# Kernel tuning notes

Hardware: AMD Instinct MI355X
Metric: run time of the kernel (lower is better)

## Reference

```python
import jax, jax.numpy as jnp
import numpy as np

EPS = 1e-8
HIDDEN = 200


def _dsmall(n, d):
    # torch: d = d*(d>eps) + eps*(d<=eps); n/d
    return n / jnp.where(d > EPS, d, EPS)


def _mp_match(v1, v2, w):
    # v1: (B,S,H); v2: (B,S,H) or (B,H); w: (L,H) -> (B,S,L)
    wt = w.T[None, None]                      # (1,1,H,L)
    a = v1[..., None] * wt                    # (B,S,H,L)
    if v2.ndim == 2:
        v2 = jnp.broadcast_to(v2[:, None, :], v1.shape)
    b = v2[..., None] * wt                    # (B,S,H,L)
    dot = jnp.sum(a * b, axis=2)
    na = jnp.linalg.norm(a, axis=2)
    nb = jnp.linalg.norm(b, axis=2)
    return dot / jnp.maximum(na * nb, EPS)    # cosine_similarity over H


def _mp_pairwise(v1, v2, w):
    # v1: (B,S1,H); v2: (B,S2,H); w: (L,H) -> (B,S1,S2,L)
    a = v1[:, None] * w[None, :, None]        # (B,L,S1,H)
    b = v2[:, None] * w[None, :, None]        # (B,L,S2,H)
    na = jnp.linalg.norm(a, axis=3, keepdims=True)   # (B,L,S1,1)
    nb = jnp.linalg.norm(b, axis=3, keepdims=True)   # (B,L,S2,1)
    n = jnp.einsum('blph,blqh->blpq', a, b)
    d = na * jnp.swapaxes(nb, 2, 3)
    return jnp.transpose(_dsmall(n, d), (0, 2, 3, 1))


def _attention(v1, v2):
    # cosine-similarity matrix (B,S1,S2)
    n1 = jnp.linalg.norm(v1, axis=2, keepdims=True)           # (B,S1,1)
    n2 = jnp.linalg.norm(v2, axis=2, keepdims=True)           # (B,S2,1)
    a = jnp.einsum('bph,bqh->bpq', v1, v2)
    return _dsmall(a, n1 * jnp.swapaxes(n2, 1, 2))


def _matching(con_p, con_h, w1, w2, w3, w4, w5, w6, w7, w8):
    p_fw, p_bw = con_p[..., :HIDDEN], con_p[..., HIDDEN:]
    h_fw, h_bw = con_h[..., :HIDDEN], con_h[..., HIDDEN:]

    # 1) full matching
    mv_p_full_fw = _mp_match(p_fw, h_fw[:, -1, :], w1)
    mv_p_full_bw = _mp_match(p_bw, h_bw[:, 0, :], w2)
    mv_h_full_fw = _mp_match(h_fw, p_fw[:, -1, :], w1)
    mv_h_full_bw = _mp_match(h_bw, p_bw[:, 0, :], w2)

    # 2) maxpooling matching
    mv_max_fw = _mp_pairwise(p_fw, h_fw, w3)  # (B,S1,S2,L)
    mv_max_bw = _mp_pairwise(p_bw, h_bw, w4)
    mv_p_max_fw = jnp.max(mv_max_fw, axis=2)
    mv_p_max_bw = jnp.max(mv_max_bw, axis=2)
    mv_h_max_fw = jnp.max(mv_max_fw, axis=1)
    mv_h_max_bw = jnp.max(mv_max_bw, axis=1)

    # 3) attentive matching (mean)
    att_fw = _attention(p_fw, h_fw)           # (B,S1,S2)
    att_bw = _attention(p_bw, h_bw)

    # sum of att_h over dim 2 is a matmul (same math, no (B,S1,S2,H) tensor)
    att_h_sum_fw = jnp.einsum('bpq,bqh->bph', att_fw, h_fw)
    att_h_sum_bw = jnp.einsum('bpq,bqh->bph', att_bw, h_bw)
    att_p_sum_fw = jnp.einsum('bpq,bph->bqh', att_fw, p_fw)
    att_p_sum_bw = jnp.einsum('bpq,bph->bqh', att_bw, p_bw)

    att_mean_h_fw = _dsmall(att_h_sum_fw, jnp.sum(att_fw, axis=2, keepdims=True))
    att_mean_h_bw = _dsmall(att_h_sum_bw, jnp.sum(att_bw, axis=2, keepdims=True))
    att_mean_p_fw = _dsmall(att_p_sum_fw, jnp.swapaxes(jnp.sum(att_fw, axis=1, keepdims=True), 1, 2))
    att_mean_p_bw = _dsmall(att_p_sum_bw, jnp.swapaxes(jnp.sum(att_bw, axis=1, keepdims=True), 1, 2))

    mv_p_att_mean_fw = _mp_match(p_fw, att_mean_h_fw, w5)
    mv_p_att_mean_bw = _mp_match(p_bw, att_mean_h_bw, w6)
    mv_h_att_mean_fw = _mp_match(h_fw, att_mean_p_fw, w5)
    mv_h_att_mean_bw = _mp_match(h_bw, att_mean_p_bw, w6)

    # 4) max-attentive matching (needs full (B,S1,S2,H) broadcast for the max)
    att_h_fw = h_fw[:, None, :, :] * att_fw[:, :, :, None]   # (B,S1,S2,H)
    att_h_bw = h_bw[:, None, :, :] * att_bw[:, :, :, None]
    att_p_fw = p_fw[:, :, None, :] * att_fw[:, :, :, None]
    att_p_bw = p_bw[:, :, None, :] * att_bw[:, :, :, None]

    att_max_h_fw = jnp.max(att_h_fw, axis=2)                 # (B,S1,H)
    att_max_h_bw = jnp.max(att_h_bw, axis=2)
    att_max_p_fw = jnp.max(att_p_fw, axis=1)                 # (B,S2,H)
    att_max_p_bw = jnp.max(att_p_bw, axis=1)

    mv_p_att_max_fw = _mp_match(p_fw, att_max_h_fw, w7)
    mv_p_att_max_bw = _mp_match(p_bw, att_max_h_bw, w8)
    mv_h_att_max_fw = _mp_match(h_fw, att_max_p_fw, w7)
    mv_h_att_max_bw = _mp_match(h_bw, att_max_p_bw, w8)

    mv_p = jnp.concatenate([mv_p_full_fw, mv_p_max_fw, mv_p_att_mean_fw, mv_p_att_max_fw,
                            mv_p_full_bw, mv_p_max_bw, mv_p_att_mean_bw, mv_p_att_max_bw], axis=2)
    mv_h = jnp.concatenate([mv_h_full_fw, mv_h_max_fw, mv_h_att_mean_fw, mv_h_att_max_fw,
                            mv_h_full_bw, mv_h_max_bw, mv_h_att_mean_bw, mv_h_att_max_bw], axis=2)
    # dropout is identity in inference mode
    return mv_p, mv_h


def setup_inputs() -> dict:
    key = jax.random.key(0)
    ks = jax.random.split(key, 10)
    B, S, H, L = 32, 64, HIDDEN, 20
    w_std = np.sqrt(2.0 / H)  # kaiming_normal fan_in
    inp = {
        'con_p': jax.random.normal(ks[0], (B, S, 2 * H), dtype=jnp.float32),
        'con_h': jax.random.normal(ks[1], (B, S, 2 * H), dtype=jnp.float32),
    }
    for i in range(8):
        inp[f'mp_w{i+1}'] = jax.random.normal(ks[2 + i], (L, H), dtype=jnp.float32) * w_std
    return inp


def reference(con_p, con_h, mp_w1, mp_w2, mp_w3, mp_w4, mp_w5, mp_w6, mp_w7, mp_w8):
    return _matching(con_p, con_h, mp_w1, mp_w2, mp_w3, mp_w4, mp_w5, mp_w6, mp_w7, mp_w8)
```

## Files before the change

kernel.cpp:

```cpp
#include <hip/hip_runtime.h>
#include <hip/hip_bf16.h>
#include <math.h>

#define EPS 1e-8f
#define BB 32
#define SS 64
#define HH 200
#define LL 20
#define KP 224
#define KST 232
#define MST 204
#define SST 68

typedef short bf16x8 __attribute__((ext_vector_type(8)));
typedef float f32x4 __attribute__((ext_vector_type(4)));

__device__ inline float bf2f(short u) {
    union { unsigned int i; float f; } v;
    v.i = ((unsigned int)(unsigned short)u) << 16;
    return v.f;
}


__global__ __launch_bounds__(512) void fused1_kernel(
        const float* __restrict__ conp, const float* __restrict__ conh,
        const float* __restrict__ w3, const float* __restrict__ w4,
        float* __restrict__ wn, float* __restrict__ meanv, float* __restrict__ maxv) {
    __shared__ __align__(16) float smem[13440];
    int t = threadIdx.x;

    if (blockIdx.x < 256) {
        float* w2L = smem;
        float* x2L = smem + 4080;
        int wnb = blockIdx.x;
        int sh = wnb & 1, sdb = wnb >> 1;
        int b = sdb & 31, sd = sdb >> 5;
        int dir = sd & 1, side = sd >> 1;
        const float* wsrc = dir ? w4 : w3;
        for (int e = t; e < LL * 25; e += 512) {
            int l = e / 25, c = e % 25, h0 = c * 8;
            float4 u0 = *(const float4*)(wsrc + l * HH + h0);
            float4 u1 = *(const float4*)(wsrc + l * HH + h0 + 4);
            *(float4*)&w2L[l * MST + h0]     = make_float4(u0.x * u0.x, u0.y * u0.y, u0.z * u0.z, u0.w * u0.w);
            *(float4*)&w2L[l * MST + h0 + 4] = make_float4(u1.x * u1.x, u1.y * u1.y, u1.z * u1.z, u1.w * u1.w);
        }
        const float* xbase = side ? conh : conp;
        for (int e = t; e < 32 * 25; e += 512) {
            int s_ = e / 25, c = e % 25, h0 = c * 8;
            const float* xp = xbase + (b * SS + sh * 32 + s_) * (2 * HH) + dir * HH + h0;
            float4 u0 = *(const float4*)xp;
            float4 u1 = *(const float4*)(xp + 4);
            *(float4*)&x2L[s_ * MST + h0]     = make_float4(u0.x * u0.x, u0.y * u0.y, u0.z * u0.z, u0.w * u0.w);
            *(float4*)&x2L[s_ * MST + h0 + 4] = make_float4(u1.x * u1.x, u1.y * u1.y, u1.z * u1.z, u1.w * u1.w);
        }
        __syncthreads();
        for (int o = t; o < 32 * LL; o += 512) {
            int s_ = o / LL, l = o % LL;
            const float4* xp = (const float4*)&x2L[s_ * MST];
            const float4* wp = (const float4*)&w2L[l * MST];
            float a0 = 0.f, a1 = 0.f, a2 = 0.f, a3 = 0.f;
            for (int h4 = 0; h4 < 50; ++h4) {
                float4 x = xp[h4]; float4 w = wp[h4];
                a0 = fmaf(x.x, w.x, a0); a1 = fmaf(x.y, w.y, a1);
                a2 = fmaf(x.z, w.z, a2); a3 = fmaf(x.w, w.w, a3);
            }
            wn[((sd * BB + b) * SS + sh * 32 + s_) * LL + l] = sqrtf(a0 + a1 + a2 + a3);
        }
    } else {
        __hip_bfloat16* AT = (__hip_bfloat16*)smem;
        __hip_bfloat16* BT = (__hip_bfloat16*)(smem + 3712);
        float* S_L  = smem + 3712 + 7424;
        float* nrmA = S_L + 32 * SST;
        float* nrmB = nrmA + 32;
        float* dsum = nrmB + 64;

        int blk = blockIdx.x - 256;
        int sh = blk & 1;
        int sdb = blk >> 1;
        int b = sdb & 31, sd = sdb >> 5;
        int dir = sd & 1, side = sd >> 1;

        if (t < 32) nrmA[t] = 0.f;
        if (t < 64) nrmB[t] = 0.f;
        __syncthreads();

        const float* selfb = side ? conh : conp;
        const float* oppb  = side ? conp : conh;

        for (int e = t; e < 32 * 28; e += 512) {
            int sl = e / 28, ck = e % 28, k = ck * 8;
            __align__(16) __hip_bfloat16 r8[8];
            if (k < HH) {
                const float* xp = selfb + (b * SS + sh * 32 + sl) * (2 * HH) + dir * HH + k;
                float xv[8];
                *(float4*)&xv[0] = *(const float4*)xp; *(float4*)&xv[4] = *(const float4*)(xp + 4);
                float ss = 0.f;
#pragma unroll
                for (int i = 0; i < 8; ++i) { r8[i] = __float2bfloat16(xv[i]); ss = fmaf(xv[i], xv[i], ss); }
                atomicAdd(&nrmA[sl], ss);
            } else {
#pragma unroll
                for (int i = 0; i < 8; ++i) r8[i] = __float2bfloat16(0.f);
            }
            *(bf16x8*)&AT[sl * KST + k] = *(bf16x8*)r8;
        }
        for (int e = t; e < 64 * 28; e += 512) {
            int rw = e / 28, ck = e % 28, k = ck * 8;
            __align__(16) __hip_bfloat16 r8[8];
            if (k < HH) {
                const float* xp = oppb + (b * SS + rw) * (2 * HH) + dir * HH + k;
                float xv[8];
                *(float4*)&xv[0] = *(const float4*)xp; *(float4*)&xv[4] = *(const float4*)(xp + 4);
                float ss = 0.f;
#pragma unroll
                for (int i = 0; i < 8; ++i) { r8[i] = __float2bfloat16(xv[i]); ss = fmaf(xv[i], xv[i], ss); }
                atomicAdd(&nrmB[rw], ss);
            } else {
#pragma unroll
                for (int i = 0; i < 8; ++i) r8[i] = __float2bfloat16(0.f);
            }
            *(bf16x8*)&BT[rw * KST + k] = *(bf16x8*)r8;
        }
        __syncthreads();

        int wv_ = __builtin_amdgcn_readfirstlane(t >> 6);
        int lane = t & 63;
        int q = lane >> 4, c = lane & 15;
        int rt = wv_ & 1, ct = wv_ >> 1;

        f32x4 acc = (f32x4){0.f, 0.f, 0.f, 0.f};
        for (int ks = 0; ks < 7; ++ks) {
            int kb = ks * 32 + q * 8;
            bf16x8 af  = *(const bf16x8*)&AT[(rt * 16 + c) * KST + kb];
            bf16x8 bf_ = *(const bf16x8*)&BT[(ct * 16 + c) * KST + kb];
            acc = __builtin_amdgcn_mfma_f32_16x16x32_bf16(af, bf_, acc, 0, 0, 0);
        }
        {
            int col = ct * 16 + c;
            float no = sqrtf(nrmB[col]);
#pragma unroll
            for (int r = 0; r < 4; ++r) {
                int row = rt * 16 + q * 4 + r;
                float ns = sqrtf(nrmA[row]);
                S_L[row * SST + col] = acc[r] / fmaxf(ns * no, EPS);
            }
        }
        __syncthreads();

        if (t < 32) {
            float sm = 0.f;
            for (int k = 0; k < 64; ++k) sm += S_L[t * SST + k];
            dsum[t] = fmaxf(sm, EPS);
        }
        __syncthreads();

        for (int e = t; e < 32 * 25; e += 512) {
            int s = e / 25, hc = e % 25, h0 = hc * 8;
            float dsv = dsum[s];
            float ms[8], mx[8];
#pragma unroll
            for (int i = 0; i < 8; ++i) { ms[i] = 0.f; mx[i] = -INFINITY; }
            for (int k = 0; k < 64; ++k) {
                float a = S_L[s * SST + k];
                bf16x8 ov = *(const bf16x8*)&BT[k * KST + h0];
#pragma unroll
                for (int i = 0; i < 8; ++i) {
                    float tt = a * bf2f(ov[i]);
                    ms[i] += tt;
                    mx[i] = fmaxf(mx[i], tt);
                }
            }
            int obase = ((sd * BB + b) * SS + sh * 32 + s) * HH + h0;
#pragma unroll
            for (int i = 0; i < 8; ++i) ms[i] /= dsv;
            *(float4*)&meanv[obase]     = *(float4*)&ms[0];
            *(float4*)&meanv[obase + 4] = *(float4*)&ms[4];
            *(float4*)&maxv[obase]      = *(float4*)&mx[0];
            *(float4*)&maxv[obase + 4]  = *(float4*)&mx[4];
        }
    }
}

__global__ __launch_bounds__(256) void fused2_kernel(
        const float* __restrict__ conp, const float* __restrict__ conh,
        const float* __restrict__ meanv, const float* __restrict__ maxv,
        const float* __restrict__ w1, const float* __restrict__ w2,
        const float* __restrict__ w3, const float* __restrict__ w4,
        const float* __restrict__ w5, const float* __restrict__ w6,
        const float* __restrict__ w7, const float* __restrict__ w8,
        const float* __restrict__ wn, float* __restrict__ out) {
    __shared__ __align__(16) float smem[15104];
    int t = threadIdx.x;

    if (blockIdx.x < 768) {
        __hip_bfloat16* AT = (__hip_bfloat16*)smem;
        __hip_bfloat16* BT = (__hip_bfloat16*)(smem + 11136);
        int blk = blockIdx.x;
        int sh = blk & 1;
        int r_ = blk >> 1;
        int m = r_ % 3;
        int sdb = r_ / 3;
        int b = sdb & 31, sd = sdb >> 5;
        int dir = sd & 1, side = sd >> 1;

        const float* wsrc = (m == 0) ? (dir ? w2 : w1)
                          : (m == 1) ? (dir ? w6 : w5)
                                     : (dir ? w8 : w7);
        const float* xbase = side ? conh : conp;
        const float* opp   = side ? conp : conh;
        int fidx = dir ? 0 : (SS - 1);
        const float* fvr = opp + (b * SS + fidx) * (2 * HH) + dir * HH;

        for (int e = t; e < 32 * 28; e += 256) {
            int sl = e / 28, ck = e % 28;
            int k = ck * 8;
            int s = sh * 32 + sl;
            __align__(16) __hip_bfloat16 r0[8], r1[8], r2[8];
            if (k < HH) {
                const float* xp = xbase + (b * SS + s) * (2 * HH) + dir * HH + k;
                const float* yp = (m == 0) ? (fvr + k)
                                : ((m == 1 ? meanv : maxv) + ((sd * BB + b) * SS + s) * HH + k);
                float xv[8], yv[8];
                *(float4*)&xv[0] = *(const float4*)xp; *(float4*)&xv[4] = *(const float4*)(xp + 4);
                *(float4*)&yv[0] = *(const float4*)yp; *(float4*)&yv[4] = *(const float4*)(yp + 4);
#pragma unroll
                for (int i = 0; i < 8; ++i) {
                    r0[i] = __float2bfloat16(xv[i] * xv[i]);
                    r1[i] = __float2bfloat16(xv[i] * yv[i]);
                    r2[i] = __float2bfloat16(yv[i] * yv[i]);
                }
            } else {
#pragma unroll
                for (int i = 0; i < 8; ++i) {
                    r0[i] = __float2bfloat16(0.f); r1[i] = __float2bfloat16(0.f); r2[i] = __float2bfloat16(0.f);
                }
            }
            *(bf16x8*)&AT[(0 * 32 + sl) * KST + k] = *(bf16x8*)r0;
            *(bf16x8*)&AT[(1 * 32 + sl) * KST + k] = *(bf16x8*)r1;
            *(bf16x8*)&AT[(2 * 32 + sl) * KST + k] = *(bf16x8*)r2;
        }
        for (int e = t; e < 32 * 28; e += 256) {
            int l = e / 28, ck = e % 28;
            int k = ck * 8;
            __align__(16) __hip_bfloat16 wr[8];
            if (l < LL && k < HH) {
                const float* wp = wsrc + l * HH + k;
                float wv[8];
                *(float4*)&wv[0] = *(const float4*)wp; *(float4*)&wv[4] = *(const float4*)(wp + 4);
#pragma unroll
                for (int i = 0; i < 8; ++i) wr[i] = __float2bfloat16(wv[i] * wv[i]);
            } else {
#pragma unroll
                for (int i = 0; i < 8; ++i) wr[i] = __float2bfloat16(0.f);
            }
            *(bf16x8*)&BT[l * KST + k] = *(bf16x8*)wr;
        }
        __syncthreads();

        int wv_ = __builtin_amdgcn_readfirstlane(t >> 6);
        int lane = t & 63;
        int q = lane >> 4, c = lane & 15;
        int slh = wv_ >> 1, ntile = wv_ & 1;

        f32x4 accA = (f32x4){0.f, 0.f, 0.f, 0.f};
        f32x4 accD = (f32x4){0.f, 0.f, 0.f, 0.f};
        f32x4 accB = (f32x4){0.f, 0.f, 0.f, 0.f};
        for (int ks = 0; ks < 7; ++ks) {
            int kb = ks * 32 + q * 8;
            bf16x8 bf = *(const bf16x8*)&BT[(ntile * 16 + c) * KST + kb];
            bf16x8 a0 = *(const bf16x8*)&AT[(0 * 32 + slh * 16 + c) * KST + kb];
            bf16x8 a1 = *(const bf16x8*)&AT[(1 * 32 + slh * 16 + c) * KST + kb];
            bf16x8 a2 = *(const bf16x8*)&AT[(2 * 32 + slh * 16 + c) * KST + kb];
            accA = __builtin_amdgcn_mfma_f32_16x16x32_bf16(a0, bf, accA, 0, 0, 0);
            accD = __builtin_amdgcn_mfma_f32_16x16x32_bf16(a1, bf, accD, 0, 0, 0);
            accB = __builtin_amdgcn_mfma_f32_16x16x32_bf16(a2, bf, accB, 0, 0, 0);
        }

        int l = ntile * 16 + c;
        if (l < LL) {
            int chunk = (m == 0) ? 0 : (m == 1) ? 40 : 60;
#pragma unroll
            for (int r = 0; r < 4; ++r) {
                int s = sh * 32 + slh * 16 + q * 4 + r;
                float cosv = accD[r] / fmaxf(sqrtf(accA[r] * accB[r]), EPS);
                out[side * (BB * SS * 160) + (b * SS + s) * 160 + dir * 80 + chunk + l] = cosv;
            }
        }
    } else {
        __hip_bfloat16* AT = (__hip_bfloat16*)smem;
        __hip_bfloat16* BT = (__hip_bfloat16*)(smem + 7424);
        float* cmL = smem + 14848;
        int blk = blockIdx.x - 768;
        int l = blk % LL; int db = blk / LL; int b = db & 31; int dir = db >> 5;

        const float* wrow = (dir ? w4 : w3) + l * HH;
        const float* Ag = conp + dir * HH;
        const float* Bg = conh + dir * HH;

        for (int e = t; e < 64 * 28; e += 256) {
            int m = e / 28, ck = e - m * 28;
            int k = ck * 8;
            __align__(16) __hip_bfloat16 at8[8];
            __align__(16) __hip_bfloat16 bt8[8];
            if (k < HH) {
                const float* ap = Ag + (b * SS + m) * (2 * HH) + k;
                const float* bp = Bg + (b * SS + m) * (2 * HH) + k;
                const float* wp = wrow + k;
                float4 a0 = *(const float4*)ap, a1 = *(const float4*)(ap + 4);
                float4 b0 = *(const float4*)bp, b1 = *(const float4*)(bp + 4);
                float4 w0 = *(const float4*)wp, w1 = *(const float4*)(wp + 4);
                at8[0] = __float2bfloat16(a0.x * w0.x); at8[1] = __float2bfloat16(a0.y * w0.y);
                at8[2] = __float2bfloat16(a0.z * w0.z); at8[3] = __float2bfloat16(a0.w * w0.w);
                at8[4] = __float2bfloat16(a1.x * w1.x); at8[5] = __float2bfloat16(a1.y * w1.y);
                at8[6] = __float2bfloat16(a1.z * w1.z); at8[7] = __float2bfloat16(a1.w * w1.w);
                bt8[0] = __float2bfloat16(b0.x * w0.x); bt8[1] = __float2bfloat16(b0.y * w0.y);
                bt8[2] = __float2bfloat16(b0.z * w0.z); bt8[3] = __float2bfloat16(b0.w * w0.w);
                bt8[4] = __float2bfloat16(b1.x * w1.x); bt8[5] = __float2bfloat16(b1.y * w1.y);
                bt8[6] = __float2bfloat16(b1.z * w1.z); bt8[7] = __float2bfloat16(b1.w * w1.w);
            } else {
#pragma unroll
                for (int ii = 0; ii < 8; ++ii) { at8[ii] = __float2bfloat16(0.f); bt8[ii] = __float2bfloat16(0.f); }
            }
            *(bf16x8*)&AT[m * KST + k] = *(bf16x8*)at8;
            *(bf16x8*)&BT[m * KST + k] = *(bf16x8*)bt8;
        }
        __syncthreads();

        int wv_ = __builtin_amdgcn_readfirstlane(t >> 6);
        int lane = t & 63;
        int q = lane >> 4, c = lane & 15;
        int m0 = wv_ * 16;

        f32x4 acc[4];
#pragma unroll
        for (int ct = 0; ct < 4; ++ct) acc[ct] = (f32x4){0.f, 0.f, 0.f, 0.f};

        for (int ks = 0; ks < 7; ++ks) {
            int kb = ks * 32 + q * 8;
            bf16x8 af = *(const bf16x8*)&AT[(m0 + c) * KST + kb];
#pragma unroll
            for (int ct = 0; ct < 4; ++ct) {
                bf16x8 bf_ = *(const bf16x8*)&BT[(ct * 16 + c) * KST + kb];
                acc[ct] = __builtin_amdgcn_mfma_f32_16x16x32_bf16(af, bf_, acc[ct], 0, 0, 0);
            }
        }

        float na[4], nb[4];
#pragma unroll
        for (int r = 0; r < 4; ++r) {
            int i = m0 + q * 4 + r;
            na[r] = wn[(((0 * 2 + dir) * BB + b) * SS + i) * LL + l];
        }
#pragma unroll
        for (int ct = 0; ct < 4; ++ct) {
            int j = ct * 16 + c;
            nb[ct] = wn[(((1 * 2 + dir) * BB + b) * SS + j) * LL + l];
        }

        float rowm[4] = {-INFINITY, -INFINITY, -INFINITY, -INFINITY};
        float colm[4] = {-INFINITY, -INFINITY, -INFINITY, -INFINITY};
#pragma unroll
        for (int ct = 0; ct < 4; ++ct) {
#pragma unroll
            for (int r = 0; r < 4; ++r) {
                float cv = acc[ct][r] / fmaxf(na[r] * nb[ct], EPS);
                rowm[r] = fmaxf(rowm[r], cv);
                colm[ct] = fmaxf(colm[ct], cv);
            }
        }

#pragma unroll
        for (int r = 0; r < 4; ++r) {
            float v = rowm[r];
            v = fmaxf(v, __shfl_xor(v, 1, 64));
            v = fmaxf(v, __shfl_xor(v, 2, 64));
            v = fmaxf(v, __shfl_xor(v, 4, 64));
            v = fmaxf(v, __shfl_xor(v, 8, 64));
            rowm[r] = v;
        }
        if (c == 0) {
#pragma unroll
            for (int r = 0; r < 4; ++r) {
                int i = m0 + q * 4 + r;
                out[(b * SS + i) * 160 + dir * 80 + 20 + l] = rowm[r];
            }
        }

#pragma unroll
        for (int ct = 0; ct < 4; ++ct) {
            float v = colm[ct];
            v = fmaxf(v, __shfl_xor(v, 16, 64));
            v = fmaxf(v, __shfl_xor(v, 32, 64));
            colm[ct] = v;
        }
        if (q == 0) {
#pragma unroll
            for (int ct = 0; ct < 4; ++ct) cmL[wv_ * 64 + ct * 16 + c] = colm[ct];
        }
        __syncthreads();
        if (t < 64) {
            float m = fmaxf(fmaxf(cmL[t], cmL[64 + t]), fmaxf(cmL[128 + t], cmL[192 + t]));
            out[BB * SS * 160 + (b * SS + t) * 160 + dir * 80 + 20 + l] = m;
        }
    }
}

extern "C" void kernel_launch(void* const* d_in, const int* in_sizes, int n_in,
                              void* d_out, int out_size, void* d_ws, size_t ws_size,
                              hipStream_t stream) {
    const float* conp = (const float*)d_in[0];
    const float* conh = (const float*)d_in[1];
    const float* w1 = (const float*)d_in[2];
    const float* w2 = (const float*)d_in[3];
    const float* w3 = (const float*)d_in[4];
    const float* w4 = (const float*)d_in[5];
    const float* w5 = (const float*)d_in[6];
    const float* w6 = (const float*)d_in[7];
    const float* w7 = (const float*)d_in[8];
    const float* w8 = (const float*)d_in[9];
    float* out = (float*)d_out;
    float* ws  = (float*)d_ws;

    float* wn     = ws;
    float* meanv  = wn + 4 * BB * SS * LL;
    float* maxv   = meanv + 4 * BB * SS * HH;

    fused1_kernel<<<512, 512, 0, stream>>>(conp, conh, w3, w4, wn, meanv, maxv);
    fused2_kernel<<<2048, 256, 0, stream>>>(conp, conh, meanv, maxv,
                                            w1, w2, w3, w4, w5, w6, w7, w8, wn, out);
}
```

Baseline: 123.6 us.

## Fuse both kernels into one, keeping attention vectors in shared memory

Merges the two launches into a single kernel. The attention mean and max vectors now stay in LDS and feed the full, mean and max-attentive multi-perspective matches within the same block, instead of going through a global workspace. The weighted norms for the pairwise max-pooling path are now accumulated inline with LDS atomics, which removes the separate norm-computation blocks. This drops one launch and the global round trip, but LDS use grows to about 108KB per block, which cuts occupancy, and half the waves sit idle during the MFMA phases.

```diff
diff --git a/kernel.cpp b/kernel.cpp
--- a/kernel.cpp
+++ b/kernel.cpp
@@ -7,10 +7,9 @@
 #define SS 64
 #define HH 200
 #define LL 20
-#define KP 224
 #define KST 232
-#define MST 204
 #define SST 68
+#define MHS 200
 
 typedef short bf16x8 __attribute__((ext_vector_type(8)));
 typedef float f32x4 __attribute__((ext_vector_type(4)));
@@ -21,71 +20,39 @@
     return v.f;
 }
 
-
-__global__ __launch_bounds__(512) void fused1_kernel(
+__global__ __launch_bounds__(512) void fused_all_kernel(
         const float* __restrict__ conp, const float* __restrict__ conh,
+        const float* __restrict__ w1, const float* __restrict__ w2,
         const float* __restrict__ w3, const float* __restrict__ w4,
-        float* __restrict__ wn, float* __restrict__ meanv, float* __restrict__ maxv) {
-    __shared__ __align__(16) float smem[13440];
+        const float* __restrict__ w5, const float* __restrict__ w6,
+        const float* __restrict__ w7, const float* __restrict__ w8,
+        float* __restrict__ out) {
+    __shared__ __align__(16) float smem[27648];
     int t = threadIdx.x;
 
     if (blockIdx.x < 256) {
-        float* w2L = smem;
-        float* x2L = smem + 4080;
-        int wnb = blockIdx.x;
-        int sh = wnb & 1, sdb = wnb >> 1;
-        int b = sdb & 31, sd = sdb >> 5;
-        int dir = sd & 1, side = sd >> 1;
-        const float* wsrc = dir ? w4 : w3;
-        for (int e = t; e < LL * 25; e += 512) {
-            int l = e / 25, c = e % 25, h0 = c * 8;
-            float4 u0 = *(const float4*)(wsrc + l * HH + h0);
-            float4 u1 = *(const float4*)(wsrc + l * HH + h0 + 4);
-            *(float4*)&w2L[l * MST + h0]     = make_float4(u0.x * u0.x, u0.y * u0.y, u0.z * u0.z, u0.w * u0.w);
-            *(float4*)&w2L[l * MST + h0 + 4] = make_float4(u1.x * u1.x, u1.y * u1.y, u1.z * u1.z, u1.w * u1.w);
-        }
-        const float* xbase = side ? conh : conp;
-        for (int e = t; e < 32 * 25; e += 512) {
-            int s_ = e / 25, c = e % 25, h0 = c * 8;
-            const float* xp = xbase + (b * SS + sh * 32 + s_) * (2 * HH) + dir * HH + h0;
-            float4 u0 = *(const float4*)xp;
-            float4 u1 = *(const float4*)(xp + 4);
-            *(float4*)&x2L[s_ * MST + h0]     = make_float4(u0.x * u0.x, u0.y * u0.y, u0.z * u0.z, u0.w * u0.w);
-            *(float4*)&x2L[s_ * MST + h0 + 4] = make_float4(u1.x * u1.x, u1.y * u1.y, u1.z * u1.z, u1.w * u1.w);
-        }
-        __syncthreads();
-        for (int o = t; o < 32 * LL; o += 512) {
-            int s_ = o / LL, l = o % LL;
-            const float4* xp = (const float4*)&x2L[s_ * MST];
-            const float4* wp = (const float4*)&w2L[l * MST];
-            float a0 = 0.f, a1 = 0.f, a2 = 0.f, a3 = 0.f;
-            for (int h4 = 0; h4 < 50; ++h4) {
-                float4 x = xp[h4]; float4 w = wp[h4];
-                a0 = fmaf(x.x, w.x, a0); a1 = fmaf(x.y, w.y, a1);
-                a2 = fmaf(x.z, w.z, a2); a3 = fmaf(x.w, w.w, a3);
-            }
-            wn[((sd * BB + b) * SS + sh * 32 + s_) * LL + l] = sqrtf(a0 + a1 + a2 + a3);
-        }
-    } else {
         __hip_bfloat16* AT = (__hip_bfloat16*)smem;
         __hip_bfloat16* BT = (__hip_bfloat16*)(smem + 3712);
-        float* S_L  = smem + 3712 + 7424;
-        float* nrmA = S_L + 32 * SST;
+        float* S_L  = smem + 11136;
+        float* nrmA = smem + 13312;
         float* nrmB = nrmA + 32;
         float* dsum = nrmB + 64;
-
-        int blk = blockIdx.x - 256;
+        __hip_bfloat16* PB = (__hip_bfloat16*)smem;
+        __hip_bfloat16* WB = (__hip_bfloat16*)(smem + 11136);
+        float* meanL = smem + 14848;
+        float* maxL  = smem + 21248;
+
+        int blk = blockIdx.x;
         int sh = blk & 1;
         int sdb = blk >> 1;
         int b = sdb & 31, sd = sdb >> 5;
         int dir = sd & 1, side = sd >> 1;
+        const float* selfb = side ? conh : conp;
+        const float* oppb  = side ? conp : conh;
 
         if (t < 32) nrmA[t] = 0.f;
         if (t < 64) nrmB[t] = 0.f;
         __syncthreads();
-
-        const float* selfb = side ? conh : conp;
-        const float* oppb  = side ? conp : conh;
 
         for (int e = t; e < 32 * 28; e += 512) {
             int sl = e / 28, ck = e % 28, k = ck * 8;
@@ -126,16 +93,16 @@
         int wv_ = __builtin_amdgcn_readfirstlane(t >> 6);
         int lane = t & 63;
         int q = lane >> 4, c = lane & 15;
-        int rt = wv_ & 1, ct = wv_ >> 1;
-
-        f32x4 acc = (f32x4){0.f, 0.f, 0.f, 0.f};
-        for (int ks = 0; ks < 7; ++ks) {
-            int kb = ks * 32 + q * 8;
-            bf16x8 af  = *(const bf16x8*)&AT[(rt * 16 + c) * KST + kb];
-            bf16x8 bf_ = *(const bf16x8*)&BT[(ct * 16 + c) * KST + kb];
-            acc = __builtin_amdgcn_mfma_f32_16x16x32_bf16(af, bf_, acc, 0, 0, 0);
-        }
+
         {
+            int rt = wv_ & 1, ct = wv_ >> 1;
+            f32x4 acc = (f32x4){0.f, 0.f, 0.f, 0.f};
+            for (int ks = 0; ks < 7; ++ks) {
+                int kb = ks * 32 + q * 8;
+                bf16x8 af  = *(const bf16x8*)&AT[(rt * 16 + c) * KST + kb];
+                bf16x8 bf_ = *(const bf16x8*)&BT[(ct * 16 + c) * KST + kb];
+                acc = __builtin_amdgcn_mfma_f32_16x16x32_bf16(af, bf_, acc, 0, 0, 0);
+            }
             int col = ct * 16 + c;
             float no = sqrtf(nrmB[col]);
 #pragma unroll
@@ -170,134 +137,116 @@
                     mx[i] = fmaxf(mx[i], tt);
                 }
             }
-            int obase = ((sd * BB + b) * SS + sh * 32 + s) * HH + h0;
 #pragma unroll
             for (int i = 0; i < 8; ++i) ms[i] /= dsv;
-            *(float4*)&meanv[obase]     = *(float4*)&ms[0];
-            *(float4*)&meanv[obase + 4] = *(float4*)&ms[4];
-            *(float4*)&maxv[obase]      = *(float4*)&mx[0];
-            *(float4*)&maxv[obase + 4]  = *(float4*)&mx[4];
-        }
-    }
-}
-
-__global__ __launch_bounds__(256) void fused2_kernel(
-        const float* __restrict__ conp, const float* __restrict__ conh,
-        const float* __restrict__ meanv, const float* __restrict__ maxv,
-        const float* __restrict__ w1, const float* __restrict__ w2,
-        const float* __restrict__ w3, const float* __restrict__ w4,
-        const float* __restrict__ w5, const float* __restrict__ w6,
-        const float* __restrict__ w7, const float* __restrict__ w8,
-        const float* __restrict__ wn, float* __restrict__ out) {
-    __shared__ __align__(16) float smem[15104];
-    int t = threadIdx.x;
-
-    if (blockIdx.x < 768) {
-        __hip_bfloat16* AT = (__hip_bfloat16*)smem;
-        __hip_bfloat16* BT = (__hip_bfloat16*)(smem + 11136);
-        int blk = blockIdx.x;
-        int sh = blk & 1;
-        int r_ = blk >> 1;
-        int m = r_ % 3;
-        int sdb = r_ / 3;
-        int b = sdb & 31, sd = sdb >> 5;
-        int dir = sd & 1, side = sd >> 1;
-
-        const float* wsrc = (m == 0) ? (dir ? w2 : w1)
-                          : (m == 1) ? (dir ? w6 : w5)
-                                     : (dir ? w8 : w7);
-        const float* xbase = side ? conh : conp;
-        const float* opp   = side ? conp : conh;
+            *(float4*)&meanL[s * MHS + h0]     = *(float4*)&ms[0];
+            *(float4*)&meanL[s * MHS + h0 + 4] = *(float4*)&ms[4];
+            *(float4*)&maxL[s * MHS + h0]      = *(float4*)&mx[0];
+            *(float4*)&maxL[s * MHS + h0 + 4]  = *(float4*)&mx[4];
+        }
+        __syncthreads();
+
         int fidx = dir ? 0 : (SS - 1);
-        const float* fvr = opp + (b * SS + fidx) * (2 * HH) + dir * HH;
-
-        for (int e = t; e < 32 * 28; e += 256) {
-            int sl = e / 28, ck = e % 28;
-            int k = ck * 8;
-            int s = sh * 32 + sl;
-            __align__(16) __hip_bfloat16 r0[8], r1[8], r2[8];
-            if (k < HH) {
-                const float* xp = xbase + (b * SS + s) * (2 * HH) + dir * HH + k;
-                const float* yp = (m == 0) ? (fvr + k)
-                                : ((m == 1 ? meanv : maxv) + ((sd * BB + b) * SS + s) * HH + k);
-                float xv[8], yv[8];
-                *(float4*)&xv[0] = *(const float4*)xp; *(float4*)&xv[4] = *(const float4*)(xp + 4);
-                *(float4*)&yv[0] = *(const float4*)yp; *(float4*)&yv[4] = *(const float4*)(yp + 4);
-#pragma unroll
-                for (int i = 0; i < 8; ++i) {
-                    r0[i] = __float2bfloat16(xv[i] * xv[i]);
-                    r1[i] = __float2bfloat16(xv[i] * yv[i]);
-                    r2[i] = __float2bfloat16(yv[i] * yv[i]);
-                }
-            } else {
-#pragma unroll
-                for (int i = 0; i < 8; ++i) {
-                    r0[i] = __float2bfloat16(0.f); r1[i] = __float2bfloat16(0.f); r2[i] = __float2bfloat16(0.f);
-                }
-            }
-            *(bf16x8*)&AT[(0 * 32 + sl) * KST + k] = *(bf16x8*)r0;
-            *(bf16x8*)&AT[(1 * 32 + sl) * KST + k] = *(bf16x8*)r1;
-            *(bf16x8*)&AT[(2 * 32 + sl) * KST + k] = *(bf16x8*)r2;
-        }
-        for (int e = t; e < 32 * 28; e += 256) {
-            int l = e / 28, ck = e % 28;
-            int k = ck * 8;
-            __align__(16) __hip_bfloat16 wr[8];
-            if (l < LL && k < HH) {
-                const float* wp = wsrc + l * HH + k;
-                float wv[8];
-                *(float4*)&wv[0] = *(const float4*)wp; *(float4*)&wv[4] = *(const float4*)(wp + 4);
-#pragma unroll
-                for (int i = 0; i < 8; ++i) wr[i] = __float2bfloat16(wv[i] * wv[i]);
-            } else {
-#pragma unroll
-                for (int i = 0; i < 8; ++i) wr[i] = __float2bfloat16(0.f);
-            }
-            *(bf16x8*)&BT[l * KST + k] = *(bf16x8*)wr;
-        }
-        __syncthreads();
-
-        int wv_ = __builtin_amdgcn_readfirstlane(t >> 6);
-        int lane = t & 63;
-        int q = lane >> 4, c = lane & 15;
-        int slh = wv_ >> 1, ntile = wv_ & 1;
-
-        f32x4 accA = (f32x4){0.f, 0.f, 0.f, 0.f};
-        f32x4 accD = (f32x4){0.f, 0.f, 0.f, 0.f};
-        f32x4 accB = (f32x4){0.f, 0.f, 0.f, 0.f};
-        for (int ks = 0; ks < 7; ++ks) {
-            int kb = ks * 32 + q * 8;
-            bf16x8 bf = *(const bf16x8*)&BT[(ntile * 16 + c) * KST + kb];
-            bf16x8 a0 = *(const bf16x8*)&AT[(0 * 32 + slh * 16 + c) * KST + kb];
-            bf16x8 a1 = *(const bf16x8*)&AT[(1 * 32 + slh * 16 + c) * KST + kb];
-            bf16x8 a2 = *(const bf16x8*)&AT[(2 * 32 + slh * 16 + c) * KST + kb];
-            accA = __builtin_amdgcn_mfma_f32_16x16x32_bf16(a0, bf, accA, 0, 0, 0);
-            accD = __builtin_amdgcn_mfma_f32_16x16x32_bf16(a1, bf, accD, 0, 0, 0);
-            accB = __builtin_amdgcn_mfma_f32_16x16x32_bf16(a2, bf, accB, 0, 0, 0);
-        }
-
-        int l = ntile * 16 + c;
-        if (l < LL) {
-            int chunk = (m == 0) ? 0 : (m == 1) ? 40 : 60;
-#pragma unroll
-            for (int r = 0; r < 4; ++r) {
-                int s = sh * 32 + slh * 16 + q * 4 + r;
-                float cosv = accD[r] / fmaxf(sqrtf(accA[r] * accB[r]), EPS);
-                out[side * (BB * SS * 160) + (b * SS + s) * 160 + dir * 80 + chunk + l] = cosv;
-            }
+        const float* fvr = oppb + (b * SS + fidx) * (2 * HH) + dir * HH;
+        for (int m = 0; m < 3; ++m) {
+            const float* wsrc = (m == 0) ? (dir ? w2 : w1)
+                              : (m == 1) ? (dir ? w6 : w5)
+                                         : (dir ? w8 : w7);
+            for (int e = t; e < 32 * 28; e += 512) {
+                int sl = e / 28, ck = e % 28, k = ck * 8;
+                __align__(16) __hip_bfloat16 r0[8], r1[8], r2[8];
+                if (k < HH) {
+                    const float* xp = selfb + (b * SS + sh * 32 + sl) * (2 * HH) + dir * HH + k;
+                    float xv[8], yv[8];
+                    *(float4*)&xv[0] = *(const float4*)xp; *(float4*)&xv[4] = *(const float4*)(xp + 4);
+                    if (m == 0) {
+                        *(float4*)&yv[0] = *(const float4*)(fvr + k);
+                        *(float4*)&yv[4] = *(const float4*)(fvr + k + 4);
+                    } else {
+                        const float* yL = (m == 1 ? meanL : maxL) + sl * MHS + k;
+                        *(float4*)&yv[0] = *(const float4*)yL;
+                        *(float4*)&yv[4] = *(const float4*)(yL + 4);
+                    }
+#pragma unroll
+                    for (int i = 0; i < 8; ++i) {
+                        if (m == 0) r0[i] = __float2bfloat16(xv[i] * xv[i]);
+                        r1[i] = __float2bfloat16(xv[i] * yv[i]);
+                        r2[i] = __float2bfloat16(yv[i] * yv[i]);
+                    }
+                } else {
+#pragma unroll
+                    for (int i = 0; i < 8; ++i) {
+                        r0[i] = __float2bfloat16(0.f);
+                        r1[i] = __float2bfloat16(0.f);
+                        r2[i] = __float2bfloat16(0.f);
+                    }
+                }
+                if (m == 0) *(bf16x8*)&PB[(0 * 32 + sl) * KST + k] = *(bf16x8*)r0;
+                *(bf16x8*)&PB[(1 * 32 + sl) * KST + k] = *(bf16x8*)r1;
+                *(bf16x8*)&PB[(2 * 32 + sl) * KST + k] = *(bf16x8*)r2;
+            }
+            for (int e = t; e < 32 * 28; e += 512) {
+                int l_ = e / 28, ck = e % 28, k = ck * 8;
+                __align__(16) __hip_bfloat16 wr[8];
+                if (l_ < LL && k < HH) {
+                    const float* wp = wsrc + l_ * HH + k;
+                    float wv[8];
+                    *(float4*)&wv[0] = *(const float4*)wp; *(float4*)&wv[4] = *(const float4*)(wp + 4);
+#pragma unroll
+                    for (int i = 0; i < 8; ++i) wr[i] = __float2bfloat16(wv[i] * wv[i]);
+                } else {
+#pragma unroll
+                    for (int i = 0; i < 8; ++i) wr[i] = __float2bfloat16(0.f);
+                }
+                *(bf16x8*)&WB[l_ * KST + k] = *(bf16x8*)wr;
+            }
+            __syncthreads();
+
+            if (wv_ < 4) {
+                int slh = wv_ >> 1, ntile = wv_ & 1;
+                f32x4 accA = (f32x4){0.f, 0.f, 0.f, 0.f};
+                f32x4 accD = (f32x4){0.f, 0.f, 0.f, 0.f};
+                f32x4 accB = (f32x4){0.f, 0.f, 0.f, 0.f};
+                for (int ks = 0; ks < 7; ++ks) {
+                    int kb = ks * 32 + q * 8;
+                    bf16x8 bfw = *(const bf16x8*)&WB[(ntile * 16 + c) * KST + kb];
+                    bf16x8 a0 = *(const bf16x8*)&PB[(0 * 32 + slh * 16 + c) * KST + kb];
+                    bf16x8 a1 = *(const bf16x8*)&PB[(1 * 32 + slh * 16 + c) * KST + kb];
+                    bf16x8 a2 = *(const bf16x8*)&PB[(2 * 32 + slh * 16 + c) * KST + kb];
+                    accA = __builtin_amdgcn_mfma_f32_16x16x32_bf16(a0, bfw, accA, 0, 0, 0);
+                    accD = __builtin_amdgcn_mfma_f32_16x16x32_bf16(a1, bfw, accD, 0, 0, 0);
+                    accB = __builtin_amdgcn_mfma_f32_16x16x32_bf16(a2, bfw, accB, 0, 0, 0);
+                }
+                int l_ = ntile * 16 + c;
+                if (l_ < LL) {
+                    int chunk = (m == 0) ? 0 : (m == 1) ? 40 : 60;
+#pragma unroll
+                    for (int r = 0; r < 4; ++r) {
+                        int s = sh * 32 + slh * 16 + q * 4 + r;
+                        float cosv = accD[r] / fmaxf(sqrtf(accA[r] * accB[r]), EPS);
+                        out[side * (BB * SS * 160) + (b * SS + s) * 160 + dir * 80 + chunk + l_] = cosv;
+                    }
+                }
+            }
+            if (m < 2) __syncthreads();
         }
     } else {
         __hip_bfloat16* AT = (__hip_bfloat16*)smem;
         __hip_bfloat16* BT = (__hip_bfloat16*)(smem + 7424);
         float* cmL = smem + 14848;
-        int blk = blockIdx.x - 768;
+        float* nA  = smem + 15104;
+        float* nB  = smem + 15168;
+        int blk = blockIdx.x - 256;
         int l = blk % LL; int db = blk / LL; int b = db & 31; int dir = db >> 5;
 
         const float* wrow = (dir ? w4 : w3) + l * HH;
         const float* Ag = conp + dir * HH;
         const float* Bg = conh + dir * HH;
 
-        for (int e = t; e < 64 * 28; e += 256) {
+        if (t < 64) { nA[t] = 0.f; nB[t] = 0.f; }
+        __syncthreads();
+
+        for (int e = t; e < 64 * 28; e += 512) {
             int m = e / 28, ck = e - m * 28;
             int k = ck * 8;
             __align__(16) __hip_bfloat16 at8[8];
@@ -306,17 +255,22 @@
                 const float* ap = Ag + (b * SS + m) * (2 * HH) + k;
                 const float* bp = Bg + (b * SS + m) * (2 * HH) + k;
                 const float* wp = wrow + k;
-                float4 a0 = *(const float4*)ap, a1 = *(const float4*)(ap + 4);
-                float4 b0 = *(const float4*)bp, b1 = *(const float4*)(bp + 4);
-                float4 w0 = *(const float4*)wp, w1 = *(const float4*)(wp + 4);
-                at8[0] = __float2bfloat16(a0.x * w0.x); at8[1] = __float2bfloat16(a0.y * w0.y);
-                at8[2] = __float2bfloat16(a0.z * w0.z); at8[3] = __float2bfloat16(a0.w * w0.w);
-                at8[4] = __float2bfloat16(a1.x * w1.x); at8[5] = __float2bfloat16(a1.y * w1.y);
-                at8[6] = __float2bfloat16(a1.z * w1.z); at8[7] = __float2bfloat16(a1.w * w1.w);
-                bt8[0] = __float2bfloat16(b0.x * w0.x); bt8[1] = __float2bfloat16(b0.y * w0.y);
-                bt8[2] = __float2bfloat16(b0.z * w0.z); bt8[3] = __float2bfloat16(b0.w * w0.w);
-                bt8[4] = __float2bfloat16(b1.x * w1.x); bt8[5] = __float2bfloat16(b1.y * w1.y);
-                bt8[6] = __float2bfloat16(b1.z * w1.z); bt8[7] = __float2bfloat16(b1.w * w1.w);
+                float av[8], bv[8], wvv[8];
+                *(float4*)&av[0]  = *(const float4*)ap; *(float4*)&av[4]  = *(const float4*)(ap + 4);
+                *(float4*)&bv[0]  = *(const float4*)bp; *(float4*)&bv[4]  = *(const float4*)(bp + 4);
+                *(float4*)&wvv[0] = *(const float4*)wp; *(float4*)&wvv[4] = *(const float4*)(wp + 4);
+                float ssa = 0.f, ssb = 0.f;
+#pragma unroll
+                for (int i = 0; i < 8; ++i) {
+                    float aw = av[i] * wvv[i];
+                    float bw = bv[i] * wvv[i];
+                    at8[i] = __float2bfloat16(aw);
+                    bt8[i] = __float2bfloat16(bw);
+                    ssa = fmaf(aw, aw, ssa);
+                    ssb = fmaf(bw, bw, ssb);
+                }
+                atomicAdd(&nA[m], ssa);
+                atomicAdd(&nB[m], ssb);
             } else {
 #pragma unroll
                 for (int ii = 0; ii < 8; ++ii) { at8[ii] = __float2bfloat16(0.f); bt8[ii] = __float2bfloat16(0.f); }
@@ -329,78 +283,73 @@
         int wv_ = __builtin_amdgcn_readfirstlane(t >> 6);
         int lane = t & 63;
         int q = lane >> 4, c = lane & 15;
-        int m0 = wv_ * 16;
-
-        f32x4 acc[4];
-#pragma unroll
-        for (int ct = 0; ct < 4; ++ct) acc[ct] = (f32x4){0.f, 0.f, 0.f, 0.f};
-
-        for (int ks = 0; ks < 7; ++ks) {
-            int kb = ks * 32 + q * 8;
-            bf16x8 af = *(const bf16x8*)&AT[(m0 + c) * KST + kb];
+
+        if (wv_ < 4) {
+            int m0 = wv_ * 16;
+            f32x4 acc[4];
+#pragma unroll
+            for (int ct = 0; ct < 4; ++ct) acc[ct] = (f32x4){0.f, 0.f, 0.f, 0.f};
+            for (int ks = 0; ks < 7; ++ks) {
+                int kb = ks * 32 + q * 8;
+                bf16x8 af = *(const bf16x8*)&AT[(m0 + c) * KST + kb];
+#pragma unroll
+                for (int ct = 0; ct < 4; ++ct) {
+                    bf16x8 bf_ = *(const bf16x8*)&BT[(ct * 16 + c) * KST + kb];
+                    acc[ct] = __builtin_amdgcn_mfma_f32_16x16x32_bf16(af, bf_, acc[ct], 0, 0, 0);
+                }
+            }
+
+            float na[4], nb[4];
+#pragma unroll
+            for (int r = 0; r < 4; ++r) na[r] = sqrtf(nA[m0 + q * 4 + r]);
+#pragma unroll
+            for (int ct = 0; ct < 4; ++ct) nb[ct] = sqrtf(nB[ct * 16 + c]);
+
+            float rowm[4] = {-INFINITY, -INFINITY, -INFINITY, -INFINITY};
+            float colm[4] = {-INFINITY, -INFINITY, -INFINITY, -INFINITY};
 #pragma unroll
             for (int ct = 0; ct < 4; ++ct) {
-                bf16x8 bf_ = *(const bf16x8*)&BT[(ct * 16 + c) * KST + kb];
-                acc[ct] = __builtin_amdgcn_mfma_f32_16x16x32_bf16(af, bf_, acc[ct], 0, 0, 0);
-            }
-        }
-
-        float na[4], nb[4];
-#pragma unroll
-        for (int r = 0; r < 4; ++r) {
-            int i = m0 + q * 4 + r;
-            na[r] = wn[(((0 * 2 + dir) * BB + b) * SS + i) * LL + l];
-        }
-#pragma unroll
-        for (int ct = 0; ct < 4; ++ct) {
-            int j = ct * 16 + c;
-            nb[ct] = wn[(((1 * 2 + dir) * BB + b) * SS + j) * LL + l];
-        }
-
-        float rowm[4] = {-INFINITY, -INFINITY, -INFINITY, -INFINITY};
-        float colm[4] = {-INFINITY, -INFINITY, -INFINITY, -INFINITY};
-#pragma unroll
-        for (int ct = 0; ct < 4; ++ct) {
+#pragma unroll
+                for (int r = 0; r < 4; ++r) {
+                    float cv = acc[ct][r] / fmaxf(na[r] * nb[ct], EPS);
+                    rowm[r] = fmaxf(rowm[r], cv);
+                    colm[ct] = fmaxf(colm[ct], cv);
+                }
+            }
+
 #pragma unroll
             for (int r = 0; r < 4; ++r) {
-                float cv = acc[ct][r] / fmaxf(na[r] * nb[ct], EPS);
-                rowm[r] = fmaxf(rowm[r], cv);
-                colm[ct] = fmaxf(colm[ct], cv);
-            }
-        }
-
-#pragma unroll
-        for (int r = 0; r < 4; ++r) {
-            float v = rowm[r];
-            v = fmaxf(v, __shfl_xor(v, 1, 64));
-            v = fmaxf(v, __shfl_xor(v, 2, 64));
-            v = fmaxf(v, __shfl_xor(v, 4, 64));
-            v = fmaxf(v, __shfl_xor(v, 8, 64));
-            rowm[r] = v;
-        }
-        if (c == 0) {
-#pragma unroll
-            for (int r = 0; r < 4; ++r) {
-                int i = m0 + q * 4 + r;
-                out[(b * SS + i) * 160 + dir * 80 + 20 + l] = rowm[r];
-            }
-        }
-
-#pragma unroll
-        for (int ct = 0; ct < 4; ++ct) {
-            float v = colm[ct];
-            v = fmaxf(v, __shfl_xor(v, 16, 64));
-            v = fmaxf(v, __shfl_xor(v, 32, 64));
-            colm[ct] = v;
-        }
-        if (q == 0) {
-#pragma unroll
-            for (int ct = 0; ct < 4; ++ct) cmL[wv_ * 64 + ct * 16 + c] = colm[ct];
+                float v = rowm[r];
+                v = fmaxf(v, __shfl_xor(v, 1, 64));
+                v = fmaxf(v, __shfl_xor(v, 2, 64));
+                v = fmaxf(v, __shfl_xor(v, 4, 64));
+                v = fmaxf(v, __shfl_xor(v, 8, 64));
+                rowm[r] = v;
+            }
+            if (c == 0) {
+#pragma unroll
+                for (int r = 0; r < 4; ++r) {
+                    int i = m0 + q * 4 + r;
+                    out[(b * SS + i) * 160 + dir * 80 + 20 + l] = rowm[r];
+                }
+            }
+
+#pragma unroll
+            for (int ct = 0; ct < 4; ++ct) {
+                float v = colm[ct];
+                v = fmaxf(v, __shfl_xor(v, 16, 64));
+                v = fmaxf(v, __shfl_xor(v, 32, 64));
+                colm[ct] = v;
+            }
+            if (q == 0) {
+#pragma unroll
+                for (int ct = 0; ct < 4; ++ct) cmL[wv_ * 64 + ct * 16 + c] = colm[ct];
+            }
         }
         __syncthreads();
         if (t < 64) {
-            float m = fmaxf(fmaxf(cmL[t], cmL[64 + t]), fmaxf(cmL[128 + t], cmL[192 + t]));
-            out[BB * SS * 160 + (b * SS + t) * 160 + dir * 80 + 20 + l] = m;
+            float mm = fmaxf(fmaxf(cmL[t], cmL[64 + t]), fmaxf(cmL[128 + t], cmL[192 + t]));
+            out[BB * SS * 160 + (b * SS + t) * 160 + dir * 80 + 20 + l] = mm;
         }
     }
 }
@@ -419,13 +368,8 @@
     const float* w7 = (const float*)d_in[8];
     const float* w8 = (const float*)d_in[9];
     float* out = (float*)d_out;
-    float* ws  = (float*)d_ws;
-
-    float* wn     = ws;
-    float* meanv  = wn + 4 * BB * SS * LL;
-    float* maxv   = meanv + 4 * BB * SS * HH;
-
-    fused1_kernel<<<512, 512, 0, stream>>>(conp, conh, w3, w4, wn, meanv, maxv);
-    fused2_kernel<<<2048, 256, 0, stream>>>(conp, conh, meanv, maxv,
-                                            w1, w2, w3, w4, w5, w6, w7, w8, wn, out);
+    (void)d_ws; (void)ws_size;
+
+    fused_all_kernel<<<1536, 512, 0, stream>>>(conp, conh,
+                                               w1, w2, w3, w4, w5, w6, w7, w8, out);
 }
```

Measured after the change: 142.1 us. 1.15x slower.
